# Kernel optimization log

Hardware: AMD Instinct MI355X
Metric: run time of the kernel (lower is better)

## Reference

```python
import jax, jax.numpy as jnp
import numpy as np

N_NODES = 10000
N_EDGES = 100000
DIM = 768
NEG_SLOPE = 0.2  # PyG GATConv default


def gat_conv(x, src, dst, W, att_src, att_dst, bias, num_nodes):
    """Single-head PyG-style GATConv. src/dst already include self-loops."""
    h = x @ W                                  # [N, D]
    a_s = h @ att_src                          # [N]
    a_d = h @ att_dst                          # [N]
    e = jax.nn.leaky_relu(a_s[src] + a_d[dst], NEG_SLOPE)  # [E']
    # segment softmax over edges sharing the same destination node
    m = jax.ops.segment_max(e, dst, num_segments=num_nodes)  # [N]
    e = jnp.exp(e - m[dst])
    denom = jax.ops.segment_sum(e, dst, num_segments=num_nodes)  # [N]
    alpha = e / denom[dst]                     # [E']
    msg = alpha[:, None] * h[src]              # [E', D]
    out = jax.ops.segment_sum(msg, dst, num_segments=num_nodes)  # [N, D]
    return out + bias


def setup_inputs() -> dict:
    key = jax.random.key(0)
    ks = jax.random.split(key, 12)
    s = 1.0 / np.sqrt(DIM)
    inp = {
        "x": jax.random.normal(ks[0], (N_NODES, DIM), dtype=jnp.float32),
        "edge_index": jax.random.randint(ks[1], (2, N_EDGES), 0, N_NODES, dtype=jnp.int64),
        "W1": jax.random.normal(ks[2], (DIM, DIM), dtype=jnp.float32) * s,
        "att_src1": jax.random.normal(ks[3], (DIM,), dtype=jnp.float32) * s,
        "att_dst1": jax.random.normal(ks[4], (DIM,), dtype=jnp.float32) * s,
        "b1": jnp.zeros((DIM,), dtype=jnp.float32),
        "W2": jax.random.normal(ks[5], (DIM, DIM), dtype=jnp.float32) * s,
        "att_src2": jax.random.normal(ks[6], (DIM,), dtype=jnp.float32) * s,
        "att_dst2": jax.random.normal(ks[7], (DIM,), dtype=jnp.float32) * s,
        "b2": jnp.zeros((DIM,), dtype=jnp.float32),
    }
    return inp


def reference(x, edge_index, W1, att_src1, att_dst1, b1, W2, att_src2, att_dst2, b2):
    n = x.shape[0]
    # PyG GATConv default add_self_loops=True
    loops = jnp.arange(n, dtype=edge_index.dtype)
    src = jnp.concatenate([edge_index[0], loops])
    dst = jnp.concatenate([edge_index[1], loops])
    h = gat_conv(x, src, dst, W1, att_src1, att_dst1, b1, n)
    h = jax.nn.relu(h)
    # dropout p=0.0 in eval -> identity
    out = gat_conv(h, src, dst, W2, att_src2, att_dst2, b2, n)
    return out
```

## Files before the change

kernel.cpp:

```cpp
#include <hip/hip_runtime.h>

#define DIM 768
#define NEG_SLOPE 0.2f

typedef unsigned short ushort_t;
typedef short short8 __attribute__((ext_vector_type(8)));
typedef float floatx4 __attribute__((ext_vector_type(4)));

__device__ __forceinline__ ushort_t f32_to_bf16(float f) {
  unsigned int b = __float_as_uint(f);
  b += 0x7FFFu + ((b >> 16) & 1u);
  return (ushort_t)(b >> 16);
}
__device__ __forceinline__ float bf16_to_f32(ushort_t u) {
  return __uint_as_float(((unsigned int)u) << 16);
}
__device__ __forceinline__ float bf16lo(unsigned int u) {
  return __uint_as_float(u << 16);
}
__device__ __forceinline__ float bf16hi(unsigned int u) {
  return __uint_as_float(u & 0xFFFF0000u);
}
__device__ __forceinline__ unsigned int pack_bf16x2(float lo, float hi) {
  return ((unsigned int)f32_to_bf16(lo)) | (((unsigned int)f32_to_bf16(hi)) << 16);
}

__device__ __forceinline__ void gl2lds16(const ushort_t* g, ushort_t* l) {
  __builtin_amdgcn_global_load_lds(
      (const __attribute__((address_space(1))) void*)g,
      (__attribute__((address_space(3))) void*)l, 16, 0, 0);
}

__global__ __launch_bounds__(256)
void prep_kernel(const float* __restrict__ x, ushort_t* __restrict__ xb, int n4,
                 const float* __restrict__ W1, ushort_t* __restrict__ wT1,
                 const float* __restrict__ W2, ushort_t* __restrict__ wT2,
                 int* __restrict__ zbase, int nz4) {
  __shared__ ushort_t tile[64][65];
  int b = blockIdx.x;
  int t = threadIdx.x;
  if (b < 288) {
    int mat = b / 144;
    int ti = b - mat * 144;
    int tr = (ti / 12) * 64;
    int tc = (ti % 12) * 64;
    const float* W = mat ? W2 : W1;
    ushort_t* wT = mat ? wT2 : wT1;
    int lr = t >> 4, lc4 = (t & 15) * 4;
#pragma unroll
    for (int p = 0; p < 4; ++p) {
      int row = lr + p * 16;
      float4 v = *(const float4*)(W + (size_t)(tr + row) * DIM + tc + lc4);
      tile[row][lc4 + 0] = f32_to_bf16(v.x);
      tile[row][lc4 + 1] = f32_to_bf16(v.y);
      tile[row][lc4 + 2] = f32_to_bf16(v.z);
      tile[row][lc4 + 3] = f32_to_bf16(v.w);
    }
    __syncthreads();
    int n = t & 63, kb = (t >> 6) * 16;
    ushort_t tmp[16];
#pragma unroll
    for (int i = 0; i < 16; ++i) tmp[i] = tile[kb + i][n];
    ushort_t* dst = wT + (size_t)(tc + n) * DIM + tr + kb;
    *(uint4*)(dst) = *(const uint4*)(&tmp[0]);
    *(uint4*)(dst + 8) = *(const uint4*)(&tmp[8]);
  } else {
    int i = (b - 288) * 256 + t;
    if (i < n4) {
      float4 v = ((const float4*)x)[i];
      ushort4 o;
      o.x = f32_to_bf16(v.x); o.y = f32_to_bf16(v.y);
      o.z = f32_to_bf16(v.z); o.w = f32_to_bf16(v.w);
      ((ushort4*)xb)[i] = o;
    }
    if (i < nz4) {
      ((uint4*)zbase)[i] = make_uint4(0, 0, 0, 0);
    }
  }
}

__global__ void hist_kernel(const int* __restrict__ ei, int* __restrict__ deg,
                            int E, int Etot) {
  int e = blockIdx.x * 256 + threadIdx.x;
  if (e >= Etot) return;
  int d = (e < E) ? ei[E + e] : (e - E);
  atomicAdd(&deg[d], 1);
}

__global__ __launch_bounds__(1024)
void scan_kernel(const int* __restrict__ deg, int* __restrict__ rowstart,
                 int* __restrict__ cursor, int n, int etot) {
  __shared__ int sdeg[10240];
  __shared__ int part[1024];
  int tid = threadIdx.x;
  for (int i = tid; i < n; i += 1024) sdeg[i] = deg[i];
  __syncthreads();
  int chunk = ((n + 1023) / 1024) | 1;
  int lo = min(tid * chunk, n);
  int hi = min(lo + chunk, n);
  int s = 0;
  for (int i = lo; i < hi; ++i) s += sdeg[i];
  part[tid] = s;
  __syncthreads();
  for (int off = 1; off < 1024; off <<= 1) {
    int v = part[tid];
    int add = (tid >= off) ? part[tid - off] : 0;
    __syncthreads();
    part[tid] = v + add;
    __syncthreads();
  }
  int run = (tid == 0) ? 0 : part[tid - 1];
  for (int i = lo; i < hi; ++i) {
    int d = sdeg[i];
    sdeg[i] = run;
    run += d;
  }
  __syncthreads();
  for (int i = tid; i < n; i += 1024) {
    int v = sdeg[i];
    rowstart[i] = v;
    cursor[i] = v;
  }
  if (tid == 0) rowstart[n] = etot;
}

__global__ void fill_kernel(const int* __restrict__ ei, int* __restrict__ cursor,
                            int* __restrict__ col, int E, int Etot) {
  int e = blockIdx.x * 256 + threadIdx.x;
  if (e >= Etot) return;
  int s, d;
  if (e < E) { s = ei[e]; d = ei[E + e]; }
  else       { s = e - E; d = e - E; }
  int pos = atomicAdd(&cursor[d], 1);
  col[pos] = s;
}

__global__ __launch_bounds__(256)
void gemm_kernel(const ushort_t* __restrict__ A, const ushort_t* __restrict__ Bt,
                 const float* __restrict__ att_s, const float* __restrict__ att_d,
                 float* __restrict__ a_s, float* __restrict__ a_d,
                 ushort_t* __restrict__ Hb, int M, int MBLK) {
  const int K = DIM;
  __shared__ __align__(16) ushort_t As[64 * 64];
  __shared__ __align__(16) ushort_t Bs[128 * 64];
  int b = blockIdx.x;
  int x = b & 7, sidx = b >> 3;
  int m_local = sidx / 6, nblk = sidx - m_local * 6;
  int mblk = x * MBLK + m_local;
  if (mblk * 64 >= M) return;
  int m0 = mblk * 64, n0 = nblk * 128;
  int tid = threadIdx.x;
  int wave = tid >> 6, lane = tid & 63;
  int quad = lane >> 4, l16 = lane & 15;
  int wn = wave * 32;

  floatx4 acc[4][2];
  const floatx4 fzero = {0.f, 0.f, 0.f, 0.f};
#pragma unroll
  for (int i = 0; i < 4; ++i)
#pragma unroll
    for (int j = 0; j < 2; ++j) acc[i][j] = fzero;

  int lr = lane >> 3, lc = lane & 7;
  const ushort_t* gA[2];
  const ushort_t* gB[4];
  ushort_t* lA[2];
  ushort_t* lB[4];
#pragma unroll
  for (int t = 0; t < 2; ++t) {
    int r = t * 32 + wave * 8 + lr;
    int g = lc ^ (r & 7);
    gA[t] = A + (size_t)min(m0 + r, M - 1) * K + g * 8;
    lA[t] = As + (t * 32 + wave * 8) * 64;
  }
#pragma unroll
  for (int t = 0; t < 4; ++t) {
    int r = t * 32 + wave * 8 + lr;
    int g = lc ^ (r & 7);
    gB[t] = Bt + (size_t)(n0 + r) * K + g * 8;
    lB[t] = Bs + (t * 32 + wave * 8) * 64;
  }

  for (int k0 = 0; k0 < K; k0 += 64) {
#pragma unroll
    for (int t = 0; t < 2; ++t) gl2lds16(gA[t] + k0, lA[t]);
#pragma unroll
    for (int t = 0; t < 4; ++t) gl2lds16(gB[t] + k0, lB[t]);
    __syncthreads();

#pragma unroll
    for (int h = 0; h < 2; ++h) {
      short8 af[4], bfr[2];
#pragma unroll
      for (int i = 0; i < 4; ++i) {
        int ra = i * 16 + l16;
        af[i] = *(const short8*)(As + ra * 64 + ((((h << 2) | quad)) ^ (ra & 7)) * 8);
      }
#pragma unroll
      for (int j = 0; j < 2; ++j) {
        int rb = wn + j * 16 + l16;
        bfr[j] = *(const short8*)(Bs + rb * 64 + ((((h << 2) | quad)) ^ (rb & 7)) * 8);
      }
#pragma unroll
      for (int i = 0; i < 4; ++i)
#pragma unroll
        for (int j = 0; j < 2; ++j)
          acc[i][j] = __builtin_amdgcn_mfma_f32_16x16x32_bf16(af[i], bfr[j], acc[i][j], 0, 0, 0);
    }
    __syncthreads();
  }

  float avs[2], avd[2];
#pragma unroll
  for (int j = 0; j < 2; ++j) {
    int c = n0 + wn + j * 16 + l16;
    avs[j] = att_s[c];
    avd[j] = att_d[c];
  }

#pragma unroll
  for (int i = 0; i < 4; ++i) {
#pragma unroll
    for (int r2 = 0; r2 < 4; ++r2) {
      int row = m0 + i * 16 + quad * 4 + r2;
      bool valid = row < M;
      float pvs = 0.f, pvd = 0.f;
#pragma unroll
      for (int j = 0; j < 2; ++j) {
        float v = acc[i][j][r2];
        if (valid) Hb[(size_t)row * DIM + n0 + wn + j * 16 + l16] = f32_to_bf16(v);
        pvs = fmaf(v, avs[j], pvs);
        pvd = fmaf(v, avd[j], pvd);
      }
#pragma unroll
      for (int off = 1; off < 16; off <<= 1) {
        pvs += __shfl_xor(pvs, off, 64);
        pvd += __shfl_xor(pvd, off, 64);
      }
      if (valid && l16 == 0) {
        atomicAdd(a_s + row, pvs);
        atomicAdd(a_d + row, pvd);
      }
    }
  }
}

__global__ __launch_bounds__(256)
void aggregate_kernel(const ushort_t* __restrict__ h, const float* __restrict__ a_s,
                      const float* __restrict__ a_d, const int* __restrict__ rowstart,
                      const int* __restrict__ col, const float* __restrict__ bias,
                      float* __restrict__ out_f32, ushort_t* __restrict__ out_bf16,
                      int relu_mode, int N) {
  int wave = threadIdx.x >> 6, lane = threadIdx.x & 63;
  int node = blockIdx.x * 4 + wave;
  if (node >= N) return;
  int start = rowstart[node], end = rowstart[node + 1];
  float ad = a_d[node];

  float vmax = -3.4e38f;
  for (int e = start + lane; e < end; e += 64) {
    float v = a_s[col[e]] + ad;
    v = (v > 0.f) ? v : NEG_SLOPE * v;
    vmax = fmaxf(vmax, v);
  }
#pragma unroll
  for (int off = 32; off > 0; off >>= 1) vmax = fmaxf(vmax, __shfl_xor(vmax, off, 64));

  float ssum = 0.f;
  for (int e = start + lane; e < end; e += 64) {
    float v = a_s[col[e]] + ad;
    v = (v > 0.f) ? v : NEG_SLOPE * v;
    ssum += __expf(v - vmax);
  }
#pragma unroll
  for (int off = 32; off > 0; off >>= 1) ssum += __shfl_xor(ssum, off, 64);
  float inv = 1.f / ssum;

  float acc8[8];
  float acc4[4];
#pragma unroll
  for (int k = 0; k < 8; ++k) acc8[k] = 0.f;
#pragma unroll
  for (int k = 0; k < 4; ++k) acc4[k] = 0.f;

  for (int base = start; base < end; base += 64) {
    int e = base + lane;
    float al = 0.f;
    int sc = 0;
    if (e < end) {
      sc = col[e];
      float v = a_s[sc] + ad;
      v = (v > 0.f) ? v : NEG_SLOPE * v;
      al = __expf(v - vmax) * inv;
    }
    int cnt = min(64, end - base);
    float w = __shfl(al, 0, 64);
    int s = __shfl(sc, 0, 64);
    const ushort_t* hr = h + (size_t)s * DIM;
    uint4 u = *(const uint4*)(hr + lane * 8);
    ushort4 t4 = *(const ushort4*)(hr + 512 + lane * 4);
    for (int j = 0; j < cnt; ++j) {
      float wn_ = 0.f;
      uint4 un;
      ushort4 tn;
      if (j + 1 < cnt) {
        wn_ = __shfl(al, j + 1, 64);
        int sn = __shfl(sc, j + 1, 64);
        const ushort_t* hrn = h + (size_t)sn * DIM;
        un = *(const uint4*)(hrn + lane * 8);
        tn = *(const ushort4*)(hrn + 512 + lane * 4);
      }
      acc8[0] = fmaf(w, bf16lo(u.x), acc8[0]);
      acc8[1] = fmaf(w, bf16hi(u.x), acc8[1]);
      acc8[2] = fmaf(w, bf16lo(u.y), acc8[2]);
      acc8[3] = fmaf(w, bf16hi(u.y), acc8[3]);
      acc8[4] = fmaf(w, bf16lo(u.z), acc8[4]);
      acc8[5] = fmaf(w, bf16hi(u.z), acc8[5]);
      acc8[6] = fmaf(w, bf16lo(u.w), acc8[6]);
      acc8[7] = fmaf(w, bf16hi(u.w), acc8[7]);
      acc4[0] = fmaf(w, bf16_to_f32(t4.x), acc4[0]);
      acc4[1] = fmaf(w, bf16_to_f32(t4.y), acc4[1]);
      acc4[2] = fmaf(w, bf16_to_f32(t4.z), acc4[2]);
      acc4[3] = fmaf(w, bf16_to_f32(t4.w), acc4[3]);
      if (j + 1 < cnt) { w = wn_; u = un; t4 = tn; }
    }
  }

  size_t ob = (size_t)node * DIM;
  int c8 = lane * 8, c4 = 512 + lane * 4;
  float4 b0 = *(const float4*)(bias + c8);
  float4 b1 = *(const float4*)(bias + c8 + 4);
  float4 b2 = *(const float4*)(bias + c4);
  float o[12];
  o[0] = acc8[0] + b0.x; o[1] = acc8[1] + b0.y;
  o[2] = acc8[2] + b0.z; o[3] = acc8[3] + b0.w;
  o[4] = acc8[4] + b1.x; o[5] = acc8[5] + b1.y;
  o[6] = acc8[6] + b1.z; o[7] = acc8[7] + b1.w;
  o[8] = acc4[0] + b2.x; o[9] = acc4[1] + b2.y;
  o[10] = acc4[2] + b2.z; o[11] = acc4[3] + b2.w;
  if (relu_mode) {
#pragma unroll
    for (int k = 0; k < 12; ++k) o[k] = fmaxf(o[k], 0.f);
    uint4 s0;
    s0.x = pack_bf16x2(o[0], o[1]);
    s0.y = pack_bf16x2(o[2], o[3]);
    s0.z = pack_bf16x2(o[4], o[5]);
    s0.w = pack_bf16x2(o[6], o[7]);
    *(uint4*)(out_bf16 + ob + c8) = s0;
    uint2 s1;
    s1.x = pack_bf16x2(o[8], o[9]);
    s1.y = pack_bf16x2(o[10], o[11]);
    *(uint2*)(out_bf16 + ob + c4) = s1;
  } else {
    *(float4*)(out_f32 + ob + c8) = make_float4(o[0], o[1], o[2], o[3]);
    *(float4*)(out_f32 + ob + c8 + 4) = make_float4(o[4], o[5], o[6], o[7]);
    *(float4*)(out_f32 + ob + c4) = make_float4(o[8], o[9], o[10], o[11]);
  }
}

extern "C" void kernel_launch(void* const* d_in, const int* in_sizes, int n_in,
                              void* d_out, int out_size, void* d_ws, size_t ws_size,
                              hipStream_t stream) {
  const float* x   = (const float*)d_in[0];
  const int*   ei  = (const int*)d_in[1];
  const float* W1  = (const float*)d_in[2];
  const float* as1 = (const float*)d_in[3];
  const float* ad1 = (const float*)d_in[4];
  const float* b1  = (const float*)d_in[5];
  const float* W2  = (const float*)d_in[6];
  const float* as2 = (const float*)d_in[7];
  const float* ad2 = (const float*)d_in[8];
  const float* b2  = (const float*)d_in[9];

  const int N = in_sizes[0] / DIM;
  const int E = in_sizes[1] / 2;
  const int Etot = E + N;

  char* p = (char*)d_ws;
  auto alloc = [&](size_t bytes) {
    char* q = p;
    p += (bytes + 255) & ~(size_t)255;
    return q;
  };
  ushort_t* Hb     = (ushort_t*)alloc((size_t)N * DIM * 2);
  ushort_t* xb     = (ushort_t*)alloc((size_t)N * DIM * 2);
  ushort_t* wT1    = (ushort_t*)alloc((size_t)DIM * DIM * 2);
  ushort_t* wT2    = (ushort_t*)alloc((size_t)DIM * DIM * 2);
  int*      zbase  = (int*)alloc((size_t)5 * N * 4 + 16);
  int*      deg    = zbase;
  float*    a_s1   = (float*)(zbase + N);
  float*    a_d1   = (float*)(zbase + 2 * N);
  float*    a_s2   = (float*)(zbase + 3 * N);
  float*    a_d2   = (float*)(zbase + 4 * N);
  int*      rowst  = (int*)alloc((size_t)(N + 1) * 4);
  int*      cursor = (int*)alloc((size_t)N * 4);
  int*      col    = (int*)alloc((size_t)Etot * 4);

  int n4 = N * DIM / 4;
  int nz4 = (5 * N + 3) / 4;
  int prep_blocks = 288 + (n4 + 255) / 256;
  prep_kernel<<<prep_blocks, 256, 0, stream>>>(x, xb, n4, W1, wT1, W2, wT2,
                                               zbase, nz4);
  hist_kernel<<<(Etot + 255) / 256, 256, 0, stream>>>(ei, deg, E, Etot);
  scan_kernel<<<1, 1024, 0, stream>>>(deg, rowst, cursor, N, Etot);
  fill_kernel<<<(Etot + 255) / 256, 256, 0, stream>>>(ei, cursor, col, E, Etot);

  int MB = (N + 63) / 64;
  int MBLK = (MB + 7) / 8;
  int gemm_blocks = 8 * MBLK * 6;
  int agg_blocks = (N + 3) / 4;

  gemm_kernel<<<gemm_blocks, 256, 0, stream>>>(xb, wT1, as1, ad1, a_s1, a_d1, Hb, N, MBLK);
  aggregate_kernel<<<agg_blocks, 256, 0, stream>>>(Hb, a_s1, a_d1, rowst, col, b1,
                                                   nullptr, xb, 1, N);
  gemm_kernel<<<gemm_blocks, 256, 0, stream>>>(xb, wT2, as2, ad2, a_s2, a_d2, Hb, N, MBLK);
  aggregate_kernel<<<agg_blocks, 256, 0, stream>>>(Hb, a_s2, a_d2, rowst, col, b2,
                                                   (float*)d_out, nullptr, 0, N);
}
```

Baseline: 231.9 us.

## Precompute W·att vectors, fuse attention scores into prep/aggregate, widen GEMM K-tile

Attention logits are now computed as x·(W·att) using precomputed W·att vectors, instead of atomics in the GEMM epilogue. Layer 1 gets them from a GEMV fused into the fill kernel, and layer 2 gets them inside the layer-1 aggregate epilogue. The histogram is merged into the prep kernel, the zero-init is replaced with a memset, and the GEMM K-tile doubles to 128 with 16-way swizzling, halving the number of barriers. The aggregate broadcasts edge weight and index pairs through LDS instead of shuffles. The changes remove atomics and one launch but add LDS pressure in the GEMM and slightly change rounding.

```diff
diff --git a/kernel.cpp b/kernel.cpp
--- a/kernel.cpp
+++ b/kernel.cpp
@@ -35,11 +35,14 @@
 void prep_kernel(const float* __restrict__ x, ushort_t* __restrict__ xb, int n4,
                  const float* __restrict__ W1, ushort_t* __restrict__ wT1,
                  const float* __restrict__ W2, ushort_t* __restrict__ wT2,
-                 int* __restrict__ zbase, int nz4) {
-  __shared__ ushort_t tile[64][65];
+                 const float* __restrict__ as1, const float* __restrict__ ad1,
+                 const float* __restrict__ as2, const float* __restrict__ ad2,
+                 float* __restrict__ wvec,
+                 const int* __restrict__ ei, int* __restrict__ deg, int E, int Etot) {
   int b = blockIdx.x;
   int t = threadIdx.x;
   if (b < 288) {
+    __shared__ ushort_t tile[64][65];
     int mat = b / 144;
     int ti = b - mat * 144;
     int tr = (ti / 12) * 64;
@@ -64,8 +67,26 @@
     ushort_t* dst = wT + (size_t)(tc + n) * DIM + tr + kb;
     *(uint4*)(dst) = *(const uint4*)(&tmp[0]);
     *(uint4*)(dst + 8) = *(const uint4*)(&tmp[8]);
+  } else if (b < 294) {
+    int idx = b - 288;
+    int l = idx / 3, nb = idx - l * 3;
+    int i = nb * 256 + t;
+    const float* W = l ? W2 : W1;
+    const float* avs = l ? as2 : as1;
+    const float* avd = l ? ad2 : ad1;
+    const float* Wrow = W + (size_t)i * DIM;
+    float ss = 0.f, dd = 0.f;
+    for (int j = 0; j < DIM; j += 4) {
+      float4 w = *(const float4*)(Wrow + j);
+      float4 vs = *(const float4*)(avs + j);
+      float4 vd = *(const float4*)(avd + j);
+      ss += w.x * vs.x + w.y * vs.y + w.z * vs.z + w.w * vs.w;
+      dd += w.x * vd.x + w.y * vd.y + w.z * vd.z + w.w * vd.w;
+    }
+    wvec[l * 2 * DIM + i] = ss;
+    wvec[l * 2 * DIM + DIM + i] = dd;
   } else {
-    int i = (b - 288) * 256 + t;
+    int i = (b - 294) * 256 + t;
     if (i < n4) {
       float4 v = ((const float4*)x)[i];
       ushort4 o;
@@ -73,18 +94,11 @@
       o.z = f32_to_bf16(v.z); o.w = f32_to_bf16(v.w);
       ((ushort4*)xb)[i] = o;
     }
-    if (i < nz4) {
-      ((uint4*)zbase)[i] = make_uint4(0, 0, 0, 0);
-    }
-  }
-}
-
-__global__ void hist_kernel(const int* __restrict__ ei, int* __restrict__ deg,
-                            int E, int Etot) {
-  int e = blockIdx.x * 256 + threadIdx.x;
-  if (e >= Etot) return;
-  int d = (e < E) ? ei[E + e] : (e - E);
-  atomicAdd(&deg[d], 1);
+    if (i < Etot) {
+      int d = (i < E) ? ei[E + i] : (i - E);
+      atomicAdd(&deg[d], 1);
+    }
+  }
 }
 
 __global__ __launch_bounds__(1024)
@@ -124,25 +138,53 @@
   if (tid == 0) rowstart[n] = etot;
 }
 
-__global__ void fill_kernel(const int* __restrict__ ei, int* __restrict__ cursor,
-                            int* __restrict__ col, int E, int Etot) {
-  int e = blockIdx.x * 256 + threadIdx.x;
-  if (e >= Etot) return;
-  int s, d;
-  if (e < E) { s = ei[e]; d = ei[E + e]; }
-  else       { s = e - E; d = e - E; }
-  int pos = atomicAdd(&cursor[d], 1);
-  col[pos] = s;
+__global__ __launch_bounds__(256)
+void fill_gemv_kernel(const int* __restrict__ ei, int* __restrict__ cursor,
+                      int* __restrict__ col, int E, int Etot, int FB,
+                      const ushort_t* __restrict__ xb,
+                      const float* __restrict__ w_s, const float* __restrict__ w_d,
+                      float* __restrict__ a_s, float* __restrict__ a_d, int N) {
+  int b = blockIdx.x;
+  if (b < FB) {
+    int e = b * 256 + threadIdx.x;
+    if (e >= Etot) return;
+    int s, d;
+    if (e < E) { s = ei[e]; d = ei[E + e]; }
+    else       { s = e - E; d = e - E; }
+    int pos = atomicAdd(&cursor[d], 1);
+    col[pos] = s;
+  } else {
+    int wave = threadIdx.x >> 6, lane = threadIdx.x & 63;
+    int node = (b - FB) * 4 + wave;
+    if (node >= N) return;
+    const ushort_t* xr = xb + (size_t)node * DIM;
+    float ss = 0.f, dd = 0.f;
+#pragma unroll
+    for (int q = 0; q < 3; ++q) {
+      int c = q * 256 + lane * 4;
+      ushort4 u = *(const ushort4*)(xr + c);
+      float4 vs = *(const float4*)(w_s + c);
+      float4 vd = *(const float4*)(w_d + c);
+      float x0 = bf16_to_f32(u.x), x1 = bf16_to_f32(u.y);
+      float x2 = bf16_to_f32(u.z), x3 = bf16_to_f32(u.w);
+      ss += x0 * vs.x + x1 * vs.y + x2 * vs.z + x3 * vs.w;
+      dd += x0 * vd.x + x1 * vd.y + x2 * vd.z + x3 * vd.w;
+    }
+#pragma unroll
+    for (int off = 32; off > 0; off >>= 1) {
+      ss += __shfl_xor(ss, off, 64);
+      dd += __shfl_xor(dd, off, 64);
+    }
+    if (lane == 0) { a_s[node] = ss; a_d[node] = dd; }
+  }
 }
 
 __global__ __launch_bounds__(256)
 void gemm_kernel(const ushort_t* __restrict__ A, const ushort_t* __restrict__ Bt,
-                 const float* __restrict__ att_s, const float* __restrict__ att_d,
-                 float* __restrict__ a_s, float* __restrict__ a_d,
                  ushort_t* __restrict__ Hb, int M, int MBLK) {
   const int K = DIM;
-  __shared__ __align__(16) ushort_t As[64 * 64];
-  __shared__ __align__(16) ushort_t Bs[128 * 64];
+  __shared__ __align__(16) ushort_t As[64 * 128];
+  __shared__ __align__(16) ushort_t Bs[128 * 128];
   int b = blockIdx.x;
   int x = b & 7, sidx = b >> 3;
   int m_local = sidx / 6, nblk = sidx - m_local * 6;
@@ -161,45 +203,46 @@
 #pragma unroll
     for (int j = 0; j < 2; ++j) acc[i][j] = fzero;
 
-  int lr = lane >> 3, lc = lane & 7;
-  const ushort_t* gA[2];
-  const ushort_t* gB[4];
-  ushort_t* lA[2];
-  ushort_t* lB[4];
-#pragma unroll
-  for (int t = 0; t < 2; ++t) {
-    int r = t * 32 + wave * 8 + lr;
-    int g = lc ^ (r & 7);
+  int lr = lane >> 4, lc = lane & 15;
+  const ushort_t* gA[4];
+  const ushort_t* gB[8];
+  ushort_t* lA[4];
+  ushort_t* lB[8];
+#pragma unroll
+  for (int t = 0; t < 4; ++t) {
+    int r = wave * 16 + t * 4 + lr;
+    int g = lc ^ (r & 15);
     gA[t] = A + (size_t)min(m0 + r, M - 1) * K + g * 8;
-    lA[t] = As + (t * 32 + wave * 8) * 64;
-  }
-#pragma unroll
-  for (int t = 0; t < 4; ++t) {
-    int r = t * 32 + wave * 8 + lr;
-    int g = lc ^ (r & 7);
+    lA[t] = As + (wave * 16 + t * 4) * 128;
+  }
+#pragma unroll
+  for (int t = 0; t < 8; ++t) {
+    int r = wave * 32 + t * 4 + lr;
+    int g = lc ^ (r & 15);
     gB[t] = Bt + (size_t)(n0 + r) * K + g * 8;
-    lB[t] = Bs + (t * 32 + wave * 8) * 64;
-  }
-
-  for (int k0 = 0; k0 < K; k0 += 64) {
-#pragma unroll
-    for (int t = 0; t < 2; ++t) gl2lds16(gA[t] + k0, lA[t]);
-#pragma unroll
-    for (int t = 0; t < 4; ++t) gl2lds16(gB[t] + k0, lB[t]);
+    lB[t] = Bs + (wave * 32 + t * 4) * 128;
+  }
+
+  for (int k0 = 0; k0 < K; k0 += 128) {
+#pragma unroll
+    for (int t = 0; t < 4; ++t) gl2lds16(gA[t] + k0, lA[t]);
+#pragma unroll
+    for (int t = 0; t < 8; ++t) gl2lds16(gB[t] + k0, lB[t]);
     __syncthreads();
 
 #pragma unroll
-    for (int h = 0; h < 2; ++h) {
+    for (int ks = 0; ks < 4; ++ks) {
+      int c = ks * 4 + quad;
       short8 af[4], bfr[2];
 #pragma unroll
       for (int i = 0; i < 4; ++i) {
         int ra = i * 16 + l16;
-        af[i] = *(const short8*)(As + ra * 64 + ((((h << 2) | quad)) ^ (ra & 7)) * 8);
+        af[i] = *(const short8*)(As + ra * 128 + (c ^ (ra & 15)) * 8);
       }
 #pragma unroll
       for (int j = 0; j < 2; ++j) {
         int rb = wn + j * 16 + l16;
-        bfr[j] = *(const short8*)(Bs + rb * 64 + ((((h << 2) | quad)) ^ (rb & 7)) * 8);
+        bfr[j] = *(const short8*)(Bs + rb * 128 + (c ^ (rb & 15)) * 8);
       }
 #pragma unroll
       for (int i = 0; i < 4; ++i)
@@ -210,36 +253,15 @@
     __syncthreads();
   }
 
-  float avs[2], avd[2];
-#pragma unroll
-  for (int j = 0; j < 2; ++j) {
-    int c = n0 + wn + j * 16 + l16;
-    avs[j] = att_s[c];
-    avd[j] = att_d[c];
-  }
-
 #pragma unroll
   for (int i = 0; i < 4; ++i) {
 #pragma unroll
     for (int r2 = 0; r2 < 4; ++r2) {
       int row = m0 + i * 16 + quad * 4 + r2;
-      bool valid = row < M;
-      float pvs = 0.f, pvd = 0.f;
-#pragma unroll
-      for (int j = 0; j < 2; ++j) {
-        float v = acc[i][j][r2];
-        if (valid) Hb[(size_t)row * DIM + n0 + wn + j * 16 + l16] = f32_to_bf16(v);
-        pvs = fmaf(v, avs[j], pvs);
-        pvd = fmaf(v, avd[j], pvd);
-      }
-#pragma unroll
-      for (int off = 1; off < 16; off <<= 1) {
-        pvs += __shfl_xor(pvs, off, 64);
-        pvd += __shfl_xor(pvd, off, 64);
-      }
-      if (valid && l16 == 0) {
-        atomicAdd(a_s + row, pvs);
-        atomicAdd(a_d + row, pvd);
+      if (row < M) {
+#pragma unroll
+        for (int j = 0; j < 2; ++j)
+          Hb[(size_t)row * DIM + n0 + wn + j * 16 + l16] = f32_to_bf16(acc[i][j][r2]);
       }
     }
   }
@@ -250,7 +272,10 @@
                       const float* __restrict__ a_d, const int* __restrict__ rowstart,
                       const int* __restrict__ col, const float* __restrict__ bias,
                       float* __restrict__ out_f32, ushort_t* __restrict__ out_bf16,
-                      int relu_mode, int N) {
+                      int relu_mode, int N,
+                      const float* __restrict__ ws2, const float* __restrict__ wd2,
+                      float* __restrict__ as2, float* __restrict__ ad2) {
+  __shared__ uint2 pairs[4][64];
   int wave = threadIdx.x >> 6, lane = threadIdx.x & 63;
   int node = blockIdx.x * 4 + wave;
   if (node >= N) return;
@@ -293,10 +318,11 @@
       v = (v > 0.f) ? v : NEG_SLOPE * v;
       al = __expf(v - vmax) * inv;
     }
+    pairs[wave][lane] = make_uint2(__float_as_uint(al), (unsigned int)sc);
     int cnt = min(64, end - base);
-    float w = __shfl(al, 0, 64);
-    int s = __shfl(sc, 0, 64);
-    const ushort_t* hr = h + (size_t)s * DIM;
+    uint2 p0 = pairs[wave][0];
+    float w = __uint_as_float(p0.x);
+    const ushort_t* hr = h + (size_t)p0.y * DIM;
     uint4 u = *(const uint4*)(hr + lane * 8);
     ushort4 t4 = *(const ushort4*)(hr + 512 + lane * 4);
     for (int j = 0; j < cnt; ++j) {
@@ -304,9 +330,9 @@
       uint4 un;
       ushort4 tn;
       if (j + 1 < cnt) {
-        wn_ = __shfl(al, j + 1, 64);
-        int sn = __shfl(sc, j + 1, 64);
-        const ushort_t* hrn = h + (size_t)sn * DIM;
+        uint2 pn = pairs[wave][j + 1];
+        wn_ = __uint_as_float(pn.x);
+        const ushort_t* hrn = h + (size_t)pn.y * DIM;
         un = *(const uint4*)(hrn + lane * 8);
         tn = *(const ushort4*)(hrn + 512 + lane * 4);
       }
@@ -340,7 +366,8 @@
   o[10] = acc4[2] + b2.z; o[11] = acc4[3] + b2.w;
   if (relu_mode) {
 #pragma unroll
-    for (int k = 0; k < 12; ++k) o[k] = fmaxf(o[k], 0.f);
+    for (int k = 0; k < 12; ++k)
+      o[k] = bf16_to_f32(f32_to_bf16(fmaxf(o[k], 0.f)));
     uint4 s0;
     s0.x = pack_bf16x2(o[0], o[1]);
     s0.y = pack_bf16x2(o[2], o[3]);
@@ -351,6 +378,24 @@
     s1.x = pack_bf16x2(o[8], o[9]);
     s1.y = pack_bf16x2(o[10], o[11]);
     *(uint2*)(out_bf16 + ob + c4) = s1;
+    float4 ws0 = *(const float4*)(ws2 + c8);
+    float4 ws1 = *(const float4*)(ws2 + c8 + 4);
+    float4 ws2v = *(const float4*)(ws2 + c4);
+    float4 wd0 = *(const float4*)(wd2 + c8);
+    float4 wd1 = *(const float4*)(wd2 + c8 + 4);
+    float4 wd2v = *(const float4*)(wd2 + c4);
+    float ps = o[0] * ws0.x + o[1] * ws0.y + o[2] * ws0.z + o[3] * ws0.w
+             + o[4] * ws1.x + o[5] * ws1.y + o[6] * ws1.z + o[7] * ws1.w
+             + o[8] * ws2v.x + o[9] * ws2v.y + o[10] * ws2v.z + o[11] * ws2v.w;
+    float pd = o[0] * wd0.x + o[1] * wd0.y + o[2] * wd0.z + o[3] * wd0.w
+             + o[4] * wd1.x + o[5] * wd1.y + o[6] * wd1.z + o[7] * wd1.w
+             + o[8] * wd2v.x + o[9] * wd2v.y + o[10] * wd2v.z + o[11] * wd2v.w;
+#pragma unroll
+    for (int off = 32; off > 0; off >>= 1) {
+      ps += __shfl_xor(ps, off, 64);
+      pd += __shfl_xor(pd, off, 64);
+    }
+    if (lane == 0) { as2[node] = ps; ad2[node] = pd; }
   } else {
     *(float4*)(out_f32 + ob + c8) = make_float4(o[0], o[1], o[2], o[3]);
     *(float4*)(out_f32 + ob + c8 + 4) = make_float4(o[4], o[5], o[6], o[7]);
@@ -386,34 +431,43 @@
   ushort_t* xb     = (ushort_t*)alloc((size_t)N * DIM * 2);
   ushort_t* wT1    = (ushort_t*)alloc((size_t)DIM * DIM * 2);
   ushort_t* wT2    = (ushort_t*)alloc((size_t)DIM * DIM * 2);
-  int*      zbase  = (int*)alloc((size_t)5 * N * 4 + 16);
-  int*      deg    = zbase;
-  float*    a_s1   = (float*)(zbase + N);
-  float*    a_d1   = (float*)(zbase + 2 * N);
-  float*    a_s2   = (float*)(zbase + 3 * N);
-  float*    a_d2   = (float*)(zbase + 4 * N);
+  float*    wvec   = (float*)alloc((size_t)4 * DIM * 4);
+  float*    a_s1   = (float*)alloc((size_t)N * 4);
+  float*    a_d1   = (float*)alloc((size_t)N * 4);
+  float*    a_s2   = (float*)alloc((size_t)N * 4);
+  float*    a_d2   = (float*)alloc((size_t)N * 4);
+  int*      deg    = (int*)alloc((size_t)N * 4);
   int*      rowst  = (int*)alloc((size_t)(N + 1) * 4);
   int*      cursor = (int*)alloc((size_t)N * 4);
   int*      col    = (int*)alloc((size_t)Etot * 4);
 
+  float* w_s1v = wvec;
+  float* w_d1v = wvec + DIM;
+  float* w_s2v = wvec + 2 * DIM;
+  float* w_d2v = wvec + 3 * DIM;
+
   int n4 = N * DIM / 4;
-  int nz4 = (5 * N + 3) / 4;
-  int prep_blocks = 288 + (n4 + 255) / 256;
+  hipMemsetAsync(deg, 0, (size_t)N * 4, stream);
+  int prep_blocks = 294 + (n4 + 255) / 256;
   prep_kernel<<<prep_blocks, 256, 0, stream>>>(x, xb, n4, W1, wT1, W2, wT2,
-                                               zbase, nz4);
-  hist_kernel<<<(Etot + 255) / 256, 256, 0, stream>>>(ei, deg, E, Etot);
+                                               as1, ad1, as2, ad2, wvec,
+                                               ei, deg, E, Etot);
   scan_kernel<<<1, 1024, 0, stream>>>(deg, rowst, cursor, N, Etot);
-  fill_kernel<<<(Etot + 255) / 256, 256, 0, stream>>>(ei, cursor, col, E, Etot);
+  int FB = (Etot + 255) / 256;
+  fill_gemv_kernel<<<FB + (N + 3) / 4, 256, 0, stream>>>(
+      ei, cursor, col, E, Etot, FB, xb, w_s1v, w_d1v, a_s1, a_d1, N);
 
   int MB = (N + 63) / 64;
   int MBLK = (MB + 7) / 8;
   int gemm_blocks = 8 * MBLK * 6;
   int agg_blocks = (N + 3) / 4;
 
-  gemm_kernel<<<gemm_blocks, 256, 0, stream>>>(xb, wT1, as1, ad1, a_s1, a_d1, Hb, N, MBLK);
+  gemm_kernel<<<gemm_blocks, 256, 0, stream>>>(xb, wT1, Hb, N, MBLK);
   aggregate_kernel<<<agg_blocks, 256, 0, stream>>>(Hb, a_s1, a_d1, rowst, col, b1,
-                                                   nullptr, xb, 1, N);
-  gemm_kernel<<<gemm_blocks, 256, 0, stream>>>(xb, wT2, as2, ad2, a_s2, a_d2, Hb, N, MBLK);
+                                                   nullptr, xb, 1, N,
+                                                   w_s2v, w_d2v, a_s2, a_d2);
+  gemm_kernel<<<gemm_blocks, 256, 0, stream>>>(xb, wT2, Hb, N, MBLK);
   aggregate_kernel<<<agg_blocks, 256, 0, stream>>>(Hb, a_s2, a_d2, rowst, col, b2,
-                                                   (float*)d_out, nullptr, 0, N);
-}
+                                                   (float*)d_out, nullptr, 0, N,
+                                                   nullptr, nullptr, nullptr, nullptr);
+}
```

Result: slower. 241.4 us (+4.1%).
